# Performance work log

Hardware: AMD Instinct MI355X
Metric: run time of the kernel (lower is better)

Reference implementation:

```python
import jax, jax.numpy as jnp
import numpy as np

CD_COEFF = 1.0


def setup_inputs() -> dict:
    key = jax.random.key(0)
    k1, k2 = jax.random.split(key)
    x_diff_pred = jax.random.normal(k1, (16, 2048, 3), dtype=jnp.float32)
    x_diff_target = jax.random.normal(k2, (16, 2048, 3), dtype=jnp.float32)
    return {"x_diff_pred": x_diff_pred, "x_diff_target": x_diff_target}


def _chamfer(p1, p2):
    # p1: (bs, N, 3), p2: (bs, M, 3)
    # squared pairwise distances: (bs, N, M)
    diff = p1[:, :, None, :] - p2[:, None, :, :]
    d2 = jnp.sum(diff * diff, axis=-1)
    # bidirectional min reduction
    min_p1 = jnp.min(d2, axis=2)  # (bs, N): nearest target for each pred point
    min_p2 = jnp.min(d2, axis=1)  # (bs, M): nearest pred for each target point
    return jnp.mean(min_p1) + jnp.mean(min_p2)


def reference(x_diff_pred, x_diff_target):
    cd = _chamfer(x_diff_pred, x_diff_target)
    return CD_COEFF * cd
```

## Files before the change

kernel.cpp:

```cpp
#include <hip/hip_runtime.h>


typedef float f2 __attribute__((ext_vector_type(2)));
typedef float f4 __attribute__((ext_vector_type(4)));

#define NPTS  2048
#define BATCH 16
#define NBLK  256
#define QPB   512
#define TPB   1024
#define NGRP  128

static __device__ __forceinline__ f2 pk_fma(f2 a, f2 b, f2 c) {
    f2 d;
    asm("v_pk_fma_f32 %0, %1, %2, %3" : "=v"(d) : "v"(a), "v"(b), "v"(c));
    return d;
}

__global__ __launch_bounds__(1024) void chamfer_kernel(
    const float* __restrict__ pred,
    const float* __restrict__ tgt,
    float* __restrict__ partial)
{
    const int bid = blockIdx.x;
    const int dir = bid >> 7;
    const int b   = (bid >> 3) & 15;
    const int qc  = (bid >> 1) & 3;
    const int th  = bid & 1;

    const int tid  = threadIdx.x;
    const int lane = tid & 63;
    const int w    = tid >> 6;

    const float* __restrict__ P = dir ? tgt  : pred;
    const float* __restrict__ T = dir ? pred : tgt;
    const float* Pb = P + (size_t)b * NPTS * 3;
    const float* Tb = T + (size_t)b * NPTS * 3 + (size_t)th * TPB * 3;

    __shared__ f4    t2a[TPB / 2];
    __shared__ f4    t2b[TPB / 2];
    __shared__ float smin[16][QPB];

    if (tid < TPB / 2) {
        const int jp = tid;
        const float x0 = Tb[(2 * jp) * 3 + 0];
        const float y0 = Tb[(2 * jp) * 3 + 1];
        const float z0 = Tb[(2 * jp) * 3 + 2];
        const float x1 = Tb[(2 * jp + 1) * 3 + 0];
        const float y1 = Tb[(2 * jp + 1) * 3 + 1];
        const float z1 = Tb[(2 * jp + 1) * 3 + 2];
        f4 A; A.x = x0; A.y = x1; A.z = y0; A.w = y1;
        f4 B; B.x = z0; B.y = z1;
        B.z = x0 * x0 + y0 * y0 + z0 * z0;
        B.w = x1 * x1 + y1 * y1 + z1 * z1;
        t2a[jp] = A;
        t2b[jp] = B;
    }

    f2 qx2[8], qy2[8], qz2[8];
    float pp[8], m0[8], m1[8];
    #pragma unroll
    for (int q = 0; q < 8; ++q) {
        const int qi = qc * QPB + q * 64 + lane;
        const float x = Pb[qi * 3 + 0];
        const float y = Pb[qi * 3 + 1];
        const float z = Pb[qi * 3 + 2];
        const float ax = -2.0f * x, ay = -2.0f * y, az = -2.0f * z;
        qx2[q].x = ax; qx2[q].y = ax;
        qy2[q].x = ay; qy2[q].y = ay;
        qz2[q].x = az; qz2[q].y = az;
        pp[q] = x * x + y * y + z * z;
        m0[q] = 3.4e38f;
        m1[q] = 3.4e38f;
    }

    __syncthreads();

    const int base = w * 32;
    #pragma unroll 4
    for (int jp = 0; jp < 32; jp += 2) {
        const f4 A0 = t2a[base + jp + 0];
        const f4 B0 = t2b[base + jp + 0];
        const f4 A1 = t2a[base + jp + 1];
        const f4 B1 = t2b[base + jp + 1];
        #pragma unroll
        for (int q = 0; q < 8; ++q) {
            f2 s0 = pk_fma(qx2[q], A0.lo, B0.hi);
            s0 = pk_fma(qy2[q], A0.hi, s0);
            s0 = pk_fma(qz2[q], B0.lo, s0);
            m0[q] = fminf(fminf(m0[q], s0.x), s0.y);
            f2 s1 = pk_fma(qx2[q], A1.lo, B1.hi);
            s1 = pk_fma(qy2[q], A1.hi, s1);
            s1 = pk_fma(qz2[q], B1.lo, s1);
            m1[q] = fminf(fminf(m1[q], s1.x), s1.y);
        }
    }

    #pragma unroll
    for (int q = 0; q < 8; ++q)
        smin[w][q * 64 + lane] = fminf(m0[q], m1[q]) + pp[q];
    __syncthreads();

    if (tid < QPB) {
        float v = smin[0][tid];
        #pragma unroll
        for (int ww = 1; ww < 16; ++ww)
            v = fminf(v, smin[ww][tid]);
        partial[bid * QPB + tid] = v;
    }
}

__global__ __launch_bounds__(256) void reduce1_kernel(
    const float* __restrict__ partial,
    float* __restrict__ gsum)
{
    const int g    = blockIdx.x;
    const int tid  = threadIdx.x;
    const int lane = tid & 63;
    const int w    = tid >> 6;
    __shared__ float s[4];

    const float* p0 = partial + (size_t)(2 * g) * QPB;
    const float* p1 = partial + (size_t)(2 * g + 1) * QPB;

    float acc = fminf(p0[tid], p1[tid]) + fminf(p0[tid + 256], p1[tid + 256]);
    #pragma unroll
    for (int off = 32; off > 0; off >>= 1)
        acc += __shfl_down(acc, off);
    if (lane == 0) s[w] = acc;
    __syncthreads();
    if (tid == 0)
        gsum[g] = s[0] + s[1] + s[2] + s[3];
}

__global__ __launch_bounds__(128) void reduce2_kernel(
    const float* __restrict__ gsum,
    float* __restrict__ out)
{
    const int tid  = threadIdx.x;
    const int lane = tid & 63;
    __shared__ float s[2];

    float v = gsum[tid];
    #pragma unroll
    for (int off = 32; off > 0; off >>= 1)
        v += __shfl_down(v, off);
    if (lane == 0) s[tid >> 6] = v;
    __syncthreads();
    if (tid == 0)
        out[0] = (s[0] + s[1]) * (1.0f / (float)(BATCH * NPTS));
}

extern "C" void kernel_launch(void* const* d_in, const int* in_sizes, int n_in,
                              void* d_out, int out_size, void* d_ws, size_t ws_size,
                              hipStream_t stream)
{
    const float* pred = (const float*)d_in[0];
    const float* tgt  = (const float*)d_in[1];
    float* out = (float*)d_out;
    float* partial = (float*)d_ws;
    float* gsum    = (float*)d_ws + (size_t)NBLK * QPB;

    chamfer_kernel<<<dim3(NBLK), dim3(1024), 0, stream>>>(pred, tgt, partial);
    reduce1_kernel<<<dim3(NGRP), dim3(256), 0, stream>>>(partial, gsum);
    reduce2_kernel<<<dim3(1), dim3(128), 0, stream>>>(gsum, out);
}
```

Before: 19.91 us.

## Double queries per block and use op_sel packed FMA for two queries per target pair

Blocks now hold 1024 queries and 512 targets (four target splits instead of two), and each thread keeps 16 queries packed two per register pair. It uses v_pk_fma_f32 op_sel modifiers to broadcast one query lane against a pair of targets, which drops the duplicated query registers. This raises query reuse per shared-memory target load and halves each wave's loop trip count. The reduction kernels are reworked to take the min over four partials per query with float4 loads, and the final reduce drops to a single wave. The partial buffer doubles in size, and the larger register working set could lower occupancy.

```diff
diff --git a/kernel.cpp b/kernel.cpp
--- a/kernel.cpp
+++ b/kernel.cpp
@@ -7,13 +7,20 @@
 #define NPTS  2048
 #define BATCH 16
 #define NBLK  256
-#define QPB   512
-#define TPB   1024
-#define NGRP  128
+#define QPB   1024
+#define TPB   512
+#define NQS   64
 
-static __device__ __forceinline__ f2 pk_fma(f2 a, f2 b, f2 c) {
+static __device__ __forceinline__ f2 pk_fma_lo(f2 a, f2 b, f2 c) {
     f2 d;
-    asm("v_pk_fma_f32 %0, %1, %2, %3" : "=v"(d) : "v"(a), "v"(b), "v"(c));
+    asm("v_pk_fma_f32 %0, %1, %2, %3 op_sel:[0,0,0] op_sel_hi:[0,1,1]"
+        : "=v"(d) : "v"(a), "v"(b), "v"(c));
+    return d;
+}
+static __device__ __forceinline__ f2 pk_fma_hi(f2 a, f2 b, f2 c) {
+    f2 d;
+    asm("v_pk_fma_f32 %0, %1, %2, %3 op_sel:[1,0,0] op_sel_hi:[1,1,1]"
+        : "=v"(d) : "v"(a), "v"(b), "v"(c));
     return d;
 }
 
@@ -23,10 +30,11 @@
     float* __restrict__ partial)
 {
     const int bid = blockIdx.x;
-    const int dir = bid >> 7;
-    const int b   = (bid >> 3) & 15;
-    const int qc  = (bid >> 1) & 3;
-    const int th  = bid & 1;
+    const int qs  = bid >> 2;
+    const int qt  = bid & 3;
+    const int dir = qs >> 5;
+    const int b   = (qs >> 1) & 15;
+    const int qc  = qs & 1;
 
     const int tid  = threadIdx.x;
     const int lane = tid & 63;
@@ -35,7 +43,7 @@
     const float* __restrict__ P = dir ? tgt  : pred;
     const float* __restrict__ T = dir ? pred : tgt;
     const float* Pb = P + (size_t)b * NPTS * 3;
-    const float* Tb = T + (size_t)b * NPTS * 3 + (size_t)th * TPB * 3;
+    const float* Tb = T + (size_t)b * NPTS * 3 + (size_t)qt * TPB * 3;
 
     __shared__ f4    t2a[TPB / 2];
     __shared__ f4    t2b[TPB / 2];
@@ -57,56 +65,67 @@
         t2b[jp] = B;
     }
 
-    f2 qx2[8], qy2[8], qz2[8];
-    float pp[8], m0[8], m1[8];
+    f2 qx2[8], qy2[8], qz2[8], pp2[8];
+    float m[16];
     #pragma unroll
-    for (int q = 0; q < 8; ++q) {
-        const int qi = qc * QPB + q * 64 + lane;
-        const float x = Pb[qi * 3 + 0];
-        const float y = Pb[qi * 3 + 1];
-        const float z = Pb[qi * 3 + 2];
-        const float ax = -2.0f * x, ay = -2.0f * y, az = -2.0f * z;
-        qx2[q].x = ax; qx2[q].y = ax;
-        qy2[q].x = ay; qy2[q].y = ay;
-        qz2[q].x = az; qz2[q].y = az;
-        pp[q] = x * x + y * y + z * z;
-        m0[q] = 3.4e38f;
-        m1[q] = 3.4e38f;
+    for (int i = 0; i < 8; ++i) {
+        #pragma unroll
+        for (int h = 0; h < 2; ++h) {
+            const int qi = qc * QPB + (2 * i + h) * 64 + lane;
+            const float x = Pb[qi * 3 + 0];
+            const float y = Pb[qi * 3 + 1];
+            const float z = Pb[qi * 3 + 2];
+            qx2[i][h] = -2.0f * x;
+            qy2[i][h] = -2.0f * y;
+            qz2[i][h] = -2.0f * z;
+            pp2[i][h] = x * x + y * y + z * z;
+            m[2 * i + h] = 3.4e38f;
+        }
     }
 
     __syncthreads();
 
-    const int base = w * 32;
-    #pragma unroll 4
-    for (int jp = 0; jp < 32; jp += 2) {
-        const f4 A0 = t2a[base + jp + 0];
-        const f4 B0 = t2b[base + jp + 0];
-        const f4 A1 = t2a[base + jp + 1];
-        const f4 B1 = t2b[base + jp + 1];
+    const int pbase = w * 16;
+    #pragma unroll 2
+    for (int jp = 0; jp < 16; jp += 2) {
+        const f4 A0 = t2a[pbase + jp + 0];
+        const f4 B0 = t2b[pbase + jp + 0];
+        const f4 A1 = t2a[pbase + jp + 1];
+        const f4 B1 = t2b[pbase + jp + 1];
         #pragma unroll
-        for (int q = 0; q < 8; ++q) {
-            f2 s0 = pk_fma(qx2[q], A0.lo, B0.hi);
-            s0 = pk_fma(qy2[q], A0.hi, s0);
-            s0 = pk_fma(qz2[q], B0.lo, s0);
-            m0[q] = fminf(fminf(m0[q], s0.x), s0.y);
-            f2 s1 = pk_fma(qx2[q], A1.lo, B1.hi);
-            s1 = pk_fma(qy2[q], A1.hi, s1);
-            s1 = pk_fma(qz2[q], B1.lo, s1);
-            m1[q] = fminf(fminf(m1[q], s1.x), s1.y);
+        for (int i = 0; i < 8; ++i) {
+            f2 s0 = pk_fma_lo(qx2[i], A0.lo, B0.hi);
+            s0 = pk_fma_lo(qy2[i], A0.hi, s0);
+            s0 = pk_fma_lo(qz2[i], B0.lo, s0);
+            m[2 * i] = fminf(fminf(m[2 * i], s0.x), s0.y);
+            f2 s1 = pk_fma_hi(qx2[i], A0.lo, B0.hi);
+            s1 = pk_fma_hi(qy2[i], A0.hi, s1);
+            s1 = pk_fma_hi(qz2[i], B0.lo, s1);
+            m[2 * i + 1] = fminf(fminf(m[2 * i + 1], s1.x), s1.y);
+            f2 s2 = pk_fma_lo(qx2[i], A1.lo, B1.hi);
+            s2 = pk_fma_lo(qy2[i], A1.hi, s2);
+            s2 = pk_fma_lo(qz2[i], B1.lo, s2);
+            m[2 * i] = fminf(fminf(m[2 * i], s2.x), s2.y);
+            f2 s3 = pk_fma_hi(qx2[i], A1.lo, B1.hi);
+            s3 = pk_fma_hi(qy2[i], A1.hi, s3);
+            s3 = pk_fma_hi(qz2[i], B1.lo, s3);
+            m[2 * i + 1] = fminf(fminf(m[2 * i + 1], s3.x), s3.y);
         }
     }
 
     #pragma unroll
-    for (int q = 0; q < 8; ++q)
-        smin[w][q * 64 + lane] = fminf(m0[q], m1[q]) + pp[q];
+    for (int i = 0; i < 8; ++i) {
+        smin[w][(2 * i + 0) * 64 + lane] = m[2 * i + 0] + pp2[i][0];
+        smin[w][(2 * i + 1) * 64 + lane] = m[2 * i + 1] + pp2[i][1];
+    }
     __syncthreads();
 
-    if (tid < QPB) {
+    {
         float v = smin[0][tid];
         #pragma unroll
         for (int ww = 1; ww < 16; ++ww)
             v = fminf(v, smin[ww][tid]);
-        partial[bid * QPB + tid] = v;
+        partial[(size_t)bid * QPB + tid] = v;
     }
 }
 
@@ -114,41 +133,43 @@
     const float* __restrict__ partial,
     float* __restrict__ gsum)
 {
-    const int g    = blockIdx.x;
+    const int qs   = blockIdx.x;
     const int tid  = threadIdx.x;
     const int lane = tid & 63;
     const int w    = tid >> 6;
     __shared__ float s[4];
 
-    const float* p0 = partial + (size_t)(2 * g) * QPB;
-    const float* p1 = partial + (size_t)(2 * g + 1) * QPB;
+    const float4* P4 = (const float4*)(partial + (size_t)qs * 4 * QPB);
+    const float4 v0 = P4[0 * (QPB / 4) + tid];
+    const float4 v1 = P4[1 * (QPB / 4) + tid];
+    const float4 v2 = P4[2 * (QPB / 4) + tid];
+    const float4 v3 = P4[3 * (QPB / 4) + tid];
 
-    float acc = fminf(p0[tid], p1[tid]) + fminf(p0[tid + 256], p1[tid + 256]);
+    const float mx = fminf(fminf(v0.x, v1.x), fminf(v2.x, v3.x));
+    const float my = fminf(fminf(v0.y, v1.y), fminf(v2.y, v3.y));
+    const float mz = fminf(fminf(v0.z, v1.z), fminf(v2.z, v3.z));
+    const float mw = fminf(fminf(v0.w, v1.w), fminf(v2.w, v3.w));
+    float acc = (mx + my) + (mz + mw);
+
     #pragma unroll
     for (int off = 32; off > 0; off >>= 1)
         acc += __shfl_down(acc, off);
     if (lane == 0) s[w] = acc;
     __syncthreads();
     if (tid == 0)
-        gsum[g] = s[0] + s[1] + s[2] + s[3];
+        gsum[qs] = (s[0] + s[1]) + (s[2] + s[3]);
 }
 
-__global__ __launch_bounds__(128) void reduce2_kernel(
+__global__ __launch_bounds__(64) void reduce2_kernel(
     const float* __restrict__ gsum,
     float* __restrict__ out)
 {
-    const int tid  = threadIdx.x;
-    const int lane = tid & 63;
-    __shared__ float s[2];
-
-    float v = gsum[tid];
+    float v = gsum[threadIdx.x];
     #pragma unroll
     for (int off = 32; off > 0; off >>= 1)
         v += __shfl_down(v, off);
-    if (lane == 0) s[tid >> 6] = v;
-    __syncthreads();
-    if (tid == 0)
-        out[0] = (s[0] + s[1]) * (1.0f / (float)(BATCH * NPTS));
+    if (threadIdx.x == 0)
+        out[0] = v * (1.0f / (float)(BATCH * NPTS));
 }
 
 extern "C" void kernel_launch(void* const* d_in, const int* in_sizes, int n_in,
@@ -162,6 +183,6 @@
     float* gsum    = (float*)d_ws + (size_t)NBLK * QPB;
 
     chamfer_kernel<<<dim3(NBLK), dim3(1024), 0, stream>>>(pred, tgt, partial);
-    reduce1_kernel<<<dim3(NGRP), dim3(256), 0, stream>>>(partial, gsum);
-    reduce2_kernel<<<dim3(1), dim3(128), 0, stream>>>(gsum, out);
+    reduce1_kernel<<<dim3(NQS), dim3(256), 0, stream>>>(partial, gsum);
+    reduce2_kernel<<<dim3(1), dim3(64), 0, stream>>>(gsum, out);
 }
```

Measured after the change: 25.45 us. 1.28x slower.
